# Optimization experiments

Measured on AMD Instinct MI355X. Metric: run time of the kernel, lower is better.

Reference implementation:

```python
import jax, jax.numpy as jnp
import numpy as np

B, T, DIM = 2, 2048, 2048
N_HEAD, N_GROUP = 16, 4
KV_HEAD = N_HEAD // N_GROUP
HEAD_DIM = DIM // N_HEAD


def setup_inputs() -> dict:
    key = jax.random.key(0)
    ks = jax.random.split(key, 7)
    x = jax.random.normal(ks[0], (B, T, DIM), dtype=jnp.float32)
    # rotary tables: last dim = head_dim // 2 (interleaved real/imag pairs)
    pos = jnp.arange(T, dtype=jnp.float32)[:, None]
    inv_freq = 1.0 / (10000.0 ** (jnp.arange(0, HEAD_DIM, 2, dtype=jnp.float32) / HEAD_DIM))
    angles = pos * inv_freq[None, :]  # [T, HEAD_DIM//2]
    freqs_cos = jnp.cos(angles)
    freqs_sin = jnp.sin(angles)
    scale = 0.02
    wq = jax.random.normal(ks[1], (DIM, N_HEAD * HEAD_DIM), dtype=jnp.float32) * scale
    wk = jax.random.normal(ks[2], (DIM, KV_HEAD * HEAD_DIM), dtype=jnp.float32) * scale
    wv = jax.random.normal(ks[3], (DIM, KV_HEAD * HEAD_DIM), dtype=jnp.float32) * scale
    wo = jax.random.normal(ks[4], (N_HEAD * HEAD_DIM, DIM), dtype=jnp.float32) * scale
    return {"x": x, "freqs_cos": freqs_cos, "freqs_sin": freqs_sin,
            "wq": wq, "wk": wk, "wv": wv, "wo": wo}


def _apply_rope(t, cos, sin):
    # t: [B, T, H, D]; interleaved pairs (..., -1, 2) as in torch reference
    tr = t.reshape(*t.shape[:-1], -1, 2)
    r, i = tr[..., 0], tr[..., 1]
    c = cos[None, :, None, :]  # [1, T, 1, D//2]
    s = sin[None, :, None, :]
    out = jnp.stack([r * c - i * s, r * s + i * c], axis=-1)
    return out.reshape(t.shape)


def reference(x, freqs_cos, freqs_sin, wq, wk, wv, wo):
    Bx, Tx, C = x.shape
    xq = (x @ wq).reshape(Bx, Tx, N_HEAD, HEAD_DIM)
    xk = (x @ wk).reshape(Bx, Tx, KV_HEAD, HEAD_DIM)
    xv = (x @ wv).reshape(Bx, Tx, KV_HEAD, HEAD_DIM)
    xq = _apply_rope(xq, freqs_cos, freqs_sin)
    xk = _apply_rope(xk, freqs_cos, freqs_sin)
    # repeat_kv: each kv head repeated n_group times consecutively
    xk = jnp.repeat(xk, N_GROUP, axis=2)  # [B, T, N_HEAD, D]
    xv = jnp.repeat(xv, N_GROUP, axis=2)
    scale = HEAD_DIM ** -0.5
    att = jnp.einsum('bqhd,bkhd->bhqk', xq, xk) * scale
    causal = jnp.tril(jnp.ones((Tx, Tx), dtype=bool))
    att = jnp.where(causal[None, None], att, -jnp.inf)
    att = jax.nn.softmax(att, axis=-1)
    out = jnp.einsum('bhqk,bkhd->bqhd', att, xv).reshape(Bx, Tx, N_HEAD * HEAD_DIM)
    return out @ wo
```

## Files before the change

kernel.cpp:

```cpp
#include <hip/hip_runtime.h>

#define TB 2
#define TT 2048
#define TDIM 2048
#define NHEADS 16
#define KVHEADS 4
#define HD 128

typedef unsigned short u16;
typedef unsigned int u32;
typedef __attribute__((ext_vector_type(8))) short short8;
typedef __attribute__((ext_vector_type(4))) float float4_t;

__device__ __forceinline__ float b2f(u16 u) {
    union { u32 i; float f; } v; v.i = ((u32)u) << 16; return v.f;
}
__device__ __forceinline__ u16 f2b(float f) {
    union { float f; u32 i; } v; v.f = f;
    u32 r = (v.i + 0x7FFFu + ((v.i >> 16) & 1u)) >> 16;
    return (u16)r;
}

__device__ __forceinline__ void gl_lds16(const void* g, void* l) {
    __builtin_amdgcn_global_load_lds((const __attribute__((address_space(1))) void*)g,
                                     (__attribute__((address_space(3))) void*)l, 16, 0, 0);
}

template <bool F32OUT>
__global__ __launch_bounds__(256, 3)
void gemm_bt(const u16* __restrict__ A, const u16* __restrict__ BT,
             void* __restrict__ Cv, int M, int N, int K) {
    __shared__ __align__(16) u16 As[128 * 64];
    __shared__ __align__(16) u16 Bs[128 * 64];
    const int tid  = threadIdx.x;
    const int wave = tid >> 6, lane = tid & 63;
    const int quad = lane >> 4, l16 = lane & 15;
    const int wm = wave >> 1, wn = wave & 1;
    const int row0 = blockIdx.y * 128, col0 = blockIdx.x * 128;

    float4_t acc[4][4];
#pragma unroll
    for (int i = 0; i < 4; i++)
#pragma unroll
        for (int j = 0; j < 4; j++) acc[i][j] = (float4_t){0.f, 0.f, 0.f, 0.f};

    for (int kk = 0; kk < K; kk += 64) {
        __syncthreads();
#pragma unroll
        for (int i = 0; i < 4; i++) {
            int n = i * 256 + wave * 64 + lane;
            int r = n >> 3, c = (n & 7) ^ (r & 7);
            gl_lds16(A  + (size_t)(row0 + r) * K + kk + c * 8, &As[(i * 256 + wave * 64) * 8]);
            gl_lds16(BT + (size_t)(col0 + r) * K + kk + c * 8, &Bs[(i * 256 + wave * 64) * 8]);
        }
        __syncthreads();
#pragma unroll
        for (int ks = 0; ks < 2; ks++) {
            short8 af[4], bf[4];
#pragma unroll
            for (int mt = 0; mt < 4; mt++) {
                int m = wm * 64 + mt * 16 + l16;
                af[mt] = *(const short8*)&As[(m * 8 + ((ks * 4 + quad) ^ (l16 & 7))) * 8];
            }
#pragma unroll
            for (int nt = 0; nt < 4; nt++) {
                int n = wn * 64 + nt * 16 + l16;
                bf[nt] = *(const short8*)&Bs[(n * 8 + ((ks * 4 + quad) ^ (l16 & 7))) * 8];
            }
#pragma unroll
            for (int mt = 0; mt < 4; mt++)
#pragma unroll
                for (int nt = 0; nt < 4; nt++)
                    acc[mt][nt] = __builtin_amdgcn_mfma_f32_16x16x32_bf16(
                        af[mt], bf[nt], acc[mt][nt], 0, 0, 0);
        }
    }
#pragma unroll
    for (int mt = 0; mt < 4; mt++)
#pragma unroll
        for (int nt = 0; nt < 4; nt++)
#pragma unroll
            for (int r = 0; r < 4; r++) {
                int row = row0 + wm * 64 + mt * 16 + quad * 4 + r;
                int col = col0 + wn * 64 + nt * 16 + l16;
                if (F32OUT)
                    ((float*)Cv)[(size_t)row * N + col] = acc[mt][nt][r];
                else
                    ((u16*)Cv)[(size_t)row * N + col] = f2b(acc[mt][nt][r]);
            }
}

__global__ void cvt_transpose(const float* __restrict__ in, u16* __restrict__ out,
                              int rows, int cols) {
    __shared__ u16 tile[32][33];
    int c0 = blockIdx.x * 32, r0 = blockIdx.y * 32;
    int tx = threadIdx.x & 31, ty = threadIdx.x >> 5;
#pragma unroll
    for (int i = 0; i < 4; i++)
        tile[ty + i * 8][tx] = f2b(in[(size_t)(r0 + ty + i * 8) * cols + c0 + tx]);
    __syncthreads();
#pragma unroll
    for (int i = 0; i < 4; i++)
        out[(size_t)(c0 + ty + i * 8) * rows + r0 + tx] = tile[tx][ty + i * 8];
}

__global__ void cvt_bf16(const float* __restrict__ in, u16* __restrict__ out) {
    size_t i = ((size_t)blockIdx.x * 256 + threadIdx.x) * 4;
    float4 v = *(const float4*)(in + i);
    ushort4 o;
    o.x = f2b(v.x); o.y = f2b(v.y); o.z = f2b(v.z); o.w = f2b(v.w);
    *(ushort4*)(out + i) = o;
}

__global__ void transpose_v(const u16* __restrict__ QKV, u16* __restrict__ Vt) {
    int z = blockIdx.z, b = z >> 2, kv = z & 3;
    const u16* in = QKV + (size_t)b * TT * 3072 + 2560 + kv * HD;
    u16* out = Vt + (size_t)z * HD * TT;
    __shared__ u16 tile[32][33];
    int t0 = blockIdx.x * 32, d0 = blockIdx.y * 32;
    int tx = threadIdx.x & 31, ty = threadIdx.x >> 5;
#pragma unroll
    for (int i = 0; i < 4; i++)
        tile[ty + i * 8][tx] = in[(size_t)(t0 + ty + i * 8) * 3072 + d0 + tx];
    __syncthreads();
#pragma unroll
    for (int i = 0; i < 4; i++)
        out[(size_t)(d0 + ty + i * 8) * TT + t0 + tx] = tile[tx][ty + i * 8];
}

__global__ void rope_k(u16* __restrict__ buf, const float* __restrict__ cosb,
                       const float* __restrict__ sinb, int colbase, int ncshift,
                       int rowstride) {
    size_t gid = (size_t)blockIdx.x * 256 + threadIdx.x;
    size_t e = gid * 8;
    int ncols = 1 << ncshift;
    int row = (int)(e >> ncshift);
    int col = (int)(e & (ncols - 1));
    int i0 = (col & (HD - 1)) >> 1;
    int t = row & (TT - 1);
    u16* p = buf + (size_t)row * rowstride + colbase + col;
    union { uint4 v; u16 u[8]; } d, o;
    d.v = *(const uint4*)p;
    float4 c4 = *(const float4*)(cosb + t * 64 + i0);
    float4 s4 = *(const float4*)(sinb + t * 64 + i0);
    float cc[4] = {c4.x, c4.y, c4.z, c4.w};
    float ss[4] = {s4.x, s4.y, s4.z, s4.w};
#pragma unroll
    for (int k = 0; k < 4; k++) {
        float re = b2f(d.u[2 * k]), im = b2f(d.u[2 * k + 1]);
        o.u[2 * k]     = f2b(re * cc[k] - im * ss[k]);
        o.u[2 * k + 1] = f2b(re * ss[k] + im * cc[k]);
    }
    *(uint4*)p = o.v;
}

#define PSTR 72
__global__ __launch_bounds__(256, 3)
void attn(const u16* __restrict__ QKV, const u16* __restrict__ Vt,
          u16* __restrict__ O) {
    const int g = blockIdx.x;
    const int h = blockIdx.y;
    const int b = blockIdx.z;
    const int kvh = h >> 2;
    const int tid = threadIdx.x, w = tid >> 6, lane = tid & 63;
    const int quad = lane >> 4, l16 = lane & 15;

    __shared__ __align__(16) u16 Ks[64 * 128];
    __shared__ __align__(16) u16 Vs[128 * 64];
    __shared__ __align__(16) u16 Ps[4][16 * PSTR];

    const u16* Kbase = QKV + (size_t)b * TT * 3072 + 2048 + kvh * HD;
    const u16* Vbase = Vt + (size_t)(b * 4 + kvh) * HD * TT;
    const float scale = 0.08838834764831843f;

    for (int ph = 0; ph < 2; ph++) {
        const int qb = ph ? (31 - g) : g;
        const u16* Qrow = QKV + ((size_t)b * TT + qb * 64 + w * 16 + l16) * 3072 + h * HD;
        short8 qf[4];
#pragma unroll
        for (int ks = 0; ks < 4; ks++)
            qf[ks] = *(const short8*)(Qrow + ks * 32 + quad * 8);

        float4_t o[8];
#pragma unroll
        for (int i = 0; i < 8; i++) o[i] = (float4_t){0.f, 0.f, 0.f, 0.f};
        float mi = -1e30f, li = 0.f;
        const int qg = qb * 64 + w * 16 + l16;

        for (int kt = 0; kt <= qb; kt++) {
            __syncthreads();
#pragma unroll
            for (int i = 0; i < 4; i++) {
                int n = i * 256 + w * 64 + lane;
                int r = n >> 4, c = (n & 15) ^ (r & 15);
                gl_lds16(Kbase + (size_t)(kt * 64 + r) * 3072 + c * 8,
                         &Ks[(i * 256 + w * 64) * 8]);
            }
#pragma unroll
            for (int i = 0; i < 4; i++) {
                int n = i * 256 + w * 64 + lane;
                int d = n >> 3, c = (n & 7) ^ (d & 7);
                gl_lds16(Vbase + (size_t)d * TT + kt * 64 + c * 8,
                         &Vs[(i * 256 + w * 64) * 8]);
            }
            __syncthreads();

            float4_t st[4];
#pragma unroll
            for (int nt = 0; nt < 4; nt++) st[nt] = (float4_t){0.f, 0.f, 0.f, 0.f};
#pragma unroll
            for (int ks = 0; ks < 4; ks++) {
                short8 af[4];
#pragma unroll
                for (int nt = 0; nt < 4; nt++)
                    af[nt] = *(const short8*)&Ks[((nt * 16 + l16) * 16 +
                                                  ((ks * 4 + quad) ^ l16)) * 8];
#pragma unroll
                for (int nt = 0; nt < 4; nt++)
                    st[nt] = __builtin_amdgcn_mfma_f32_16x16x32_bf16(
                        af[nt], qf[ks], st[nt], 0, 0, 0);
            }

            const bool diag = (kt == qb);
            float pm = -1e30f;
#pragma unroll
            for (int nt = 0; nt < 4; nt++)
#pragma unroll
                for (int r = 0; r < 4; r++) {
                    float v = st[nt][r] * scale;
                    int key = kt * 64 + nt * 16 + quad * 4 + r;
                    if (diag && key > qg) v = -1e30f;
                    st[nt][r] = v;
                    pm = fmaxf(pm, v);
                }
            pm = fmaxf(pm, __shfl_xor(pm, 16, 64));
            pm = fmaxf(pm, __shfl_xor(pm, 32, 64));
            float mnew = fmaxf(mi, pm);
            float alpha = __expf(mi - mnew);
            mi = mnew;
            float rs = 0.f;
#pragma unroll
            for (int nt = 0; nt < 4; nt++)
#pragma unroll
                for (int r = 0; r < 4; r++) {
                    float e = __expf(st[nt][r] - mnew);
                    st[nt][r] = e;
                    rs += e;
                }
            rs += __shfl_xor(rs, 16, 64);
            rs += __shfl_xor(rs, 32, 64);
            li = li * alpha + rs;

#pragma unroll
            for (int nt = 0; nt < 4; nt++) {
                uint2 pk;
                pk.x = (u32)f2b(st[nt][0]) | ((u32)f2b(st[nt][1]) << 16);
                pk.y = (u32)f2b(st[nt][2]) | ((u32)f2b(st[nt][3]) << 16);
                *(uint2*)&Ps[w][l16 * PSTR + nt * 16 + quad * 4] = pk;
            }
            float a_o[4];
#pragma unroll
            for (int r = 0; r < 4; r++) a_o[r] = __shfl(alpha, quad * 4 + r, 64);
#pragma unroll
            for (int n2 = 0; n2 < 8; n2++)
#pragma unroll
                for (int r = 0; r < 4; r++) o[n2][r] *= a_o[r];

#pragma unroll
            for (int ks2 = 0; ks2 < 2; ks2++) {
                short8 ap = *(const short8*)&Ps[w][l16 * PSTR + ks2 * 32 + quad * 8];
#pragma unroll
                for (int n2 = 0; n2 < 8; n2++) {
                    short8 bv = *(const short8*)&Vs[((n2 * 16 + l16) * 8 +
                                                     ((ks2 * 4 + quad) ^ (l16 & 7))) * 8];
                    o[n2] = __builtin_amdgcn_mfma_f32_16x16x32_bf16(ap, bv, o[n2], 0, 0, 0);
                }
            }
        }

        float l_o[4];
#pragma unroll
        for (int r = 0; r < 4; r++) l_o[r] = __shfl(li, quad * 4 + r, 64);
        u16* Ob2 = O + ((size_t)b * TT + qb * 64 + w * 16) * TDIM + h * HD;
#pragma unroll
        for (int n2 = 0; n2 < 8; n2++)
#pragma unroll
            for (int r = 0; r < 4; r++)
                Ob2[(size_t)(quad * 4 + r) * TDIM + n2 * 16 + l16] =
                    f2b(o[n2][r] / l_o[r]);
    }
}

extern "C" void kernel_launch(void* const* d_in, const int* in_sizes, int n_in,
                              void* d_out, int out_size, void* d_ws, size_t ws_size,
                              hipStream_t stream) {
    const float* x  = (const float*)d_in[0];
    const float* fc = (const float*)d_in[1];
    const float* fs = (const float*)d_in[2];
    const float* wq = (const float*)d_in[3];
    const float* wk = (const float*)d_in[4];
    const float* wv = (const float*)d_in[5];
    const float* wo = (const float*)d_in[6];
    float* out = (float*)d_out;

    char* ws = (char*)d_ws;
    size_t off = 0;
    auto alloc = [&](size_t bytes) -> void* {
        void* p = ws + off;
        off += (bytes + 255) & ~(size_t)255;
        return p;
    };
    u16* xb  = (u16*)alloc((size_t)4096 * 2048 * 2);
    u16* WT  = (u16*)alloc((size_t)3072 * 2048 * 2);
    u16* woT = (u16*)alloc((size_t)2048 * 2048 * 2);
    u16* QKV = (u16*)alloc((size_t)4096 * 3072 * 2);
    u16* Vtb = (u16*)alloc((size_t)4096 * 512 * 2);
    u16* Ob  = (u16*)alloc((size_t)4096 * 2048 * 2);

    dim3 blk(256);
    cvt_bf16<<<dim3(8192), blk, 0, stream>>>(x, xb);
    cvt_transpose<<<dim3(64, 64), blk, 0, stream>>>(wq, WT, 2048, 2048);
    cvt_transpose<<<dim3(16, 64), blk, 0, stream>>>(wk, WT + (size_t)2048 * 2048, 2048, 512);
    cvt_transpose<<<dim3(16, 64), blk, 0, stream>>>(wv, WT + (size_t)2560 * 2048, 2048, 512);
    cvt_transpose<<<dim3(64, 64), blk, 0, stream>>>(wo, woT, 2048, 2048);
    gemm_bt<false><<<dim3(24, 32), blk, 0, stream>>>(xb, WT, QKV, 4096, 3072, 2048);
    rope_k<<<dim3(4096), blk, 0, stream>>>(QKV, fc, fs, 0, 11, 3072);
    rope_k<<<dim3(1024), blk, 0, stream>>>(QKV, fc, fs, 2048, 9, 3072);
    transpose_v<<<dim3(64, 4, 8), blk, 0, stream>>>(QKV, Vtb);
    attn<<<dim3(16, 16, 2), blk, 0, stream>>>(QKV, Vtb, Ob);
    gemm_bt<true><<<dim3(16, 32), blk, 0, stream>>>(Ob, woT, out, 4096, 2048, 2048);
}
```

Baseline: 316.3 us.

## Double-buffer K/V tiles in attention and streamline the softmax math

The attention kernel now keeps two LDS buffers for K and V. The next key tile's async global-to-LDS load is issued before the current tile is computed, which removes the second barrier per iteration and overlaps memory latency with MFMA work. The softmax folds the 1/sqrt(d) scale and log2(e) into a single exp2 argument and applies the causal mask only on the diagonal tile. P is packed to bf16 by truncation through a byte permute instead of round-to-nearest, which costs a little precision. Doubling the LDS footprint lowers the launch-bound occupancy hint from 3 to 2 blocks, which may reduce latency hiding.

```diff
diff --git a/kernel.cpp b/kernel.cpp
--- a/kernel.cpp
+++ b/kernel.cpp
@@ -19,6 +19,9 @@
     union { float f; u32 i; } v; v.f = f;
     u32 r = (v.i + 0x7FFFu + ((v.i >> 16) & 1u)) >> 16;
     return (u16)r;
+}
+__device__ __forceinline__ u32 fbits(float f) {
+    union { float f; u32 i; } v; v.f = f; return v.i;
 }
 
 __device__ __forceinline__ void gl_lds16(const void* g, void* l) {
@@ -155,7 +158,7 @@
 }
 
 #define PSTR 72
-__global__ __launch_bounds__(256, 3)
+__global__ __launch_bounds__(256, 2)
 void attn(const u16* __restrict__ QKV, const u16* __restrict__ Vt,
           u16* __restrict__ O) {
     const int g = blockIdx.x;
@@ -165,16 +168,36 @@
     const int tid = threadIdx.x, w = tid >> 6, lane = tid & 63;
     const int quad = lane >> 4, l16 = lane & 15;
 
-    __shared__ __align__(16) u16 Ks[64 * 128];
-    __shared__ __align__(16) u16 Vs[128 * 64];
+    __shared__ __align__(16) u16 Ks[2][64 * 128];
+    __shared__ __align__(16) u16 Vs[2][128 * 64];
     __shared__ __align__(16) u16 Ps[4][16 * PSTR];
 
     const u16* Kbase = QKV + (size_t)b * TT * 3072 + 2048 + kvh * HD;
     const u16* Vbase = Vt + (size_t)(b * 4 + kvh) * HD * TT;
-    const float scale = 0.08838834764831843f;
+    const float Cl = 0.12753102474f;
+
+    auto stage = [&](int kt, int bb) {
+#pragma unroll
+        for (int i = 0; i < 4; i++) {
+            int n = i * 256 + w * 64 + lane;
+            int r = n >> 4, c = (n & 15) ^ (r & 15);
+            gl_lds16(Kbase + (size_t)(kt * 64 + r) * 3072 + c * 8,
+                     &Ks[bb][(i * 256 + w * 64) * 8]);
+        }
+#pragma unroll
+        for (int i = 0; i < 4; i++) {
+            int n = i * 256 + w * 64 + lane;
+            int d = n >> 3, c = (n & 7) ^ (d & 7);
+            gl_lds16(Vbase + (size_t)d * TT + kt * 64 + c * 8,
+                     &Vs[bb][(i * 256 + w * 64) * 8]);
+        }
+    };
 
     for (int ph = 0; ph < 2; ph++) {
         const int qb = ph ? (31 - g) : g;
+        __syncthreads();
+        stage(0, 0);
+
         const u16* Qrow = QKV + ((size_t)b * TT + qb * 64 + w * 16 + l16) * 3072 + h * HD;
         short8 qf[4];
 #pragma unroll
@@ -188,22 +211,9 @@
         const int qg = qb * 64 + w * 16 + l16;
 
         for (int kt = 0; kt <= qb; kt++) {
+            const int cur = kt & 1;
             __syncthreads();
-#pragma unroll
-            for (int i = 0; i < 4; i++) {
-                int n = i * 256 + w * 64 + lane;
-                int r = n >> 4, c = (n & 15) ^ (r & 15);
-                gl_lds16(Kbase + (size_t)(kt * 64 + r) * 3072 + c * 8,
-                         &Ks[(i * 256 + w * 64) * 8]);
-            }
-#pragma unroll
-            for (int i = 0; i < 4; i++) {
-                int n = i * 256 + w * 64 + lane;
-                int d = n >> 3, c = (n & 7) ^ (d & 7);
-                gl_lds16(Vbase + (size_t)d * TT + kt * 64 + c * 8,
-                         &Vs[(i * 256 + w * 64) * 8]);
-            }
-            __syncthreads();
+            if (kt < qb) stage(kt + 1, cur ^ 1);
 
             float4_t st[4];
 #pragma unroll
@@ -213,37 +223,40 @@
                 short8 af[4];
 #pragma unroll
                 for (int nt = 0; nt < 4; nt++)
-                    af[nt] = *(const short8*)&Ks[((nt * 16 + l16) * 16 +
-                                                  ((ks * 4 + quad) ^ l16)) * 8];
+                    af[nt] = *(const short8*)&Ks[cur][((nt * 16 + l16) * 16 +
+                                                      ((ks * 4 + quad) ^ l16)) * 8];
 #pragma unroll
                 for (int nt = 0; nt < 4; nt++)
                     st[nt] = __builtin_amdgcn_mfma_f32_16x16x32_bf16(
                         af[nt], qf[ks], st[nt], 0, 0, 0);
             }
 
-            const bool diag = (kt == qb);
-            float pm = -1e30f;
+            if (kt == qb) {
+#pragma unroll
+                for (int nt = 0; nt < 4; nt++)
+#pragma unroll
+                    for (int r = 0; r < 4; r++) {
+                        int key = kt * 64 + nt * 16 + quad * 4 + r;
+                        if (key > qg) st[nt][r] = -3e38f;
+                    }
+            }
+            float pm = -3e38f;
 #pragma unroll
             for (int nt = 0; nt < 4; nt++)
 #pragma unroll
-                for (int r = 0; r < 4; r++) {
-                    float v = st[nt][r] * scale;
-                    int key = kt * 64 + nt * 16 + quad * 4 + r;
-                    if (diag && key > qg) v = -1e30f;
-                    st[nt][r] = v;
-                    pm = fmaxf(pm, v);
-                }
+                for (int r = 0; r < 4; r++) pm = fmaxf(pm, st[nt][r]);
             pm = fmaxf(pm, __shfl_xor(pm, 16, 64));
             pm = fmaxf(pm, __shfl_xor(pm, 32, 64));
             float mnew = fmaxf(mi, pm);
-            float alpha = __expf(mi - mnew);
+            float alpha = __builtin_amdgcn_exp2f((mi - mnew) * Cl);
             mi = mnew;
+            const float mC = mnew * Cl;
             float rs = 0.f;
 #pragma unroll
             for (int nt = 0; nt < 4; nt++)
 #pragma unroll
                 for (int r = 0; r < 4; r++) {
-                    float e = __expf(st[nt][r] - mnew);
+                    float e = __builtin_amdgcn_exp2f(fmaf(st[nt][r], Cl, -mC));
                     st[nt][r] = e;
                     rs += e;
                 }
@@ -254,8 +267,8 @@
 #pragma unroll
             for (int nt = 0; nt < 4; nt++) {
                 uint2 pk;
-                pk.x = (u32)f2b(st[nt][0]) | ((u32)f2b(st[nt][1]) << 16);
-                pk.y = (u32)f2b(st[nt][2]) | ((u32)f2b(st[nt][3]) << 16);
+                pk.x = __builtin_amdgcn_perm(fbits(st[nt][1]), fbits(st[nt][0]), 0x07060302u);
+                pk.y = __builtin_amdgcn_perm(fbits(st[nt][3]), fbits(st[nt][2]), 0x07060302u);
                 *(uint2*)&Ps[w][l16 * PSTR + nt * 16 + quad * 4] = pk;
             }
             float a_o[4];
@@ -271,8 +284,8 @@
                 short8 ap = *(const short8*)&Ps[w][l16 * PSTR + ks2 * 32 + quad * 8];
 #pragma unroll
                 for (int n2 = 0; n2 < 8; n2++) {
-                    short8 bv = *(const short8*)&Vs[((n2 * 16 + l16) * 8 +
-                                                     ((ks2 * 4 + quad) ^ (l16 & 7))) * 8];
+                    short8 bv = *(const short8*)&Vs[cur][((n2 * 16 + l16) * 8 +
+                                                         ((ks2 * 4 + quad) ^ (l16 & 7))) * 8];
                     o[n2] = __builtin_amdgcn_mfma_f32_16x16x32_bf16(ap, bv, o[n2], 0, 0, 0);
                 }
             }
```

Measured after the change: 300.4 us. -5.0%, faster.
